# Optimization experiments

Measured on AMD Instinct MI355X. Metric: run time of the kernel, lower is better.

## Reference

```python
import jax, jax.numpy as jnp
import numpy as np

M0 = 0.3  # DTM mass parameter (layer init m0)
LIMS = [[-1.0, 1.0], [-1.0, 1.0]]
BY = 0.025


def _make_grid(lims, by):
    # Exact replica of tf_gridBy (including row ordering via full transpose)
    axes = [np.arange(lo, hi + by, by, dtype=np.float32) for lo, hi in lims]
    mesh = np.stack(np.meshgrid(*axes, indexing='ij'), 0)   # [d, n1, n2]
    grid = np.transpose(mesh).reshape(-1, len(lims))        # [N, d]
    return jnp.asarray(grid)


def setup_inputs() -> dict:
    key = jax.random.key(0)
    k1, k2 = jax.random.split(key)
    B, M = 2, 2048
    inputs = jax.random.normal(k1, (B, M, 2), dtype=jnp.float32)
    weight = jax.random.uniform(k2, (B, M), dtype=jnp.float32)  # positive weights
    grid = _make_grid(LIMS, BY)  # [6561, 2]
    return {"inputs": inputs, "weight": weight, "grid": grid}


def reference(inputs, weight, grid):
    # inputs: [B, M, d], weight: [B, M], grid: [N, d] -> dtm: [B, N]
    # Uses k = M (full sorted neighbor list); identical math to the original
    # data-dependent k = max(searchsorted)+1 truncation, since searchsorted
    # selects the same prefix index either way.
    wB = M0 * jnp.sum(weight, -1, keepdims=True)            # [B, 1] weightBound

    # Brute-force euclidean cdist grid -> points (tf_knn, r=2)
    X2 = jnp.sum(inputs * inputs, -1)                        # [B, M]
    G2 = jnp.sum(grid * grid, -1)                            # [N]
    XG = jnp.einsum('bmd,nd->bnm', inputs, grid)             # [B, N, M]
    dist = jnp.sqrt(jnp.maximum(G2[None, :, None] + X2[:, None, :] - 2.0 * XG, 0.0))

    # Full ascending sort = top_k with k=M (knnDistance, knnIndex)
    idx = jnp.argsort(dist, axis=-1)                         # [B, N, M]
    dsort = jnp.take_along_axis(dist, idx, axis=-1)

    # gather weights by neighbor index, cumulative mass
    wTemp = jnp.take_along_axis(jnp.broadcast_to(weight[:, None, :], idx.shape), idx, axis=-1)
    wcum = jnp.cumsum(wTemp, -1)                             # [B, N, M]

    bound = wB[..., None]                                    # [B, 1, 1]
    # searchsorted(side='left') == count of entries strictly below bound
    kidx = jnp.sum(wcum < bound, -1)                         # [B, N]

    d2 = dsort * dsort
    cumD = jnp.cumsum(d2 * wTemp, -1)
    val = cumD + d2 * (bound - wcum)                         # [B, N, M]
    sel = jnp.take_along_axis(val, kidx[..., None], axis=-1)[..., 0]  # [B, N]
    return jnp.sqrt(sel / wB)
```

## Files before the change

kernel.cpp:

```cpp
#include <hip/hip_runtime.h>
#include <math.h>


#define M_POINTS 2048
#define PER_LANE 32
#define M0 0.3f

template<int CTRL>
__device__ __forceinline__ float dpp_add_step(float x) {
    union { int i; float f; } u, r;
    u.f = x;
    r.i = __builtin_amdgcn_update_dpp(0, u.i, CTRL, 0xf, 0xf, true);
    return x + r.f;
}
template<int CTRL>
__device__ __forceinline__ float dpp_max_step(float x) {
    union { int i; float f; } u, r;
    u.f = x;
    r.i = __builtin_amdgcn_update_dpp(0, u.i, CTRL, 0xf, 0xf, true);
    return fmaxf(x, r.f);
}
template<int CTRL>
__device__ __forceinline__ float dpp_min_step(float x) {
    union { int i; float f; } u, r;
    u.f = x;
    r.i = __builtin_amdgcn_update_dpp(0x7F800000, u.i, CTRL, 0xf, 0xf, false);
    return fminf(x, r.f);
}
__device__ __forceinline__ float lane63(float x) {
    union { int i; float f; } u;
    u.f = x;
    u.i = __builtin_amdgcn_readlane(u.i, 63);
    return u.f;
}
__device__ __forceinline__ float wave_reduce_sum(float x) {
    x = dpp_add_step<0x111>(x); x = dpp_add_step<0x112>(x);
    x = dpp_add_step<0x114>(x); x = dpp_add_step<0x118>(x);
    x = dpp_add_step<0x142>(x); x = dpp_add_step<0x143>(x);
    return lane63(x);
}
__device__ __forceinline__ float wave_reduce_max(float x) {
    x = dpp_max_step<0x111>(x); x = dpp_max_step<0x112>(x);
    x = dpp_max_step<0x114>(x); x = dpp_max_step<0x118>(x);
    x = dpp_max_step<0x142>(x); x = dpp_max_step<0x143>(x);
    return lane63(x);
}
__device__ __forceinline__ float wave_reduce_min(float x) {
    x = dpp_min_step<0x111>(x); x = dpp_min_step<0x112>(x);
    x = dpp_min_step<0x114>(x); x = dpp_min_step<0x118>(x);
    x = dpp_min_step<0x142>(x); x = dpp_min_step<0x143>(x);
    return lane63(x);
}
__device__ __forceinline__ void wave_reduce_sum3(float& a, float& b, float& c) {
    a = dpp_add_step<0x111>(a); b = dpp_add_step<0x111>(b); c = dpp_add_step<0x111>(c);
    a = dpp_add_step<0x112>(a); b = dpp_add_step<0x112>(b); c = dpp_add_step<0x112>(c);
    a = dpp_add_step<0x114>(a); b = dpp_add_step<0x114>(b); c = dpp_add_step<0x114>(c);
    a = dpp_add_step<0x118>(a); b = dpp_add_step<0x118>(b); c = dpp_add_step<0x118>(c);
    a = dpp_add_step<0x142>(a); b = dpp_add_step<0x142>(b); c = dpp_add_step<0x142>(c);
    a = dpp_add_step<0x143>(a); b = dpp_add_step<0x143>(b); c = dpp_add_step<0x143>(c);
    a = lane63(a); b = lane63(b); c = lane63(c);
}

__global__ __launch_bounds__(256) void dtm_kernel(
    const float* __restrict__ inputs,
    const float* __restrict__ weight,
    const float* __restrict__ grid,
    float* __restrict__ out,
    int B, int N)
{
    const int lane = threadIdx.x & 63;
    const int gwave = blockIdx.x * (blockDim.x >> 6) + (threadIdx.x >> 6);
    if (gwave >= B * N) return;
    const int b = gwave / N;
    const int n = gwave - b * N;

    const float gx = grid[2 * n];
    const float gy = grid[2 * n + 1];

    const float* __restrict__ inb = inputs + (size_t)b * M_POINTS * 2;
    const float* __restrict__ wb  = weight + (size_t)b * M_POINTS;

    const int base = lane * PER_LANE;
    const float4* __restrict__ xyv = reinterpret_cast<const float4*>(inb + 2 * base);
    const float4* __restrict__ wv  = reinterpret_cast<const float4*>(wb + base);

    float d2[PER_LANE], w[PER_LANE];
    float wsum_local = 0.0f, vmax_local = 0.0f;
    #pragma unroll
    for (int q = 0; q < PER_LANE / 4; ++q) {
        const float4 wq = wv[q];
        const float4 a  = xyv[2 * q];
        const float4 c4 = xyv[2 * q + 1];
        float dx, dy;
        dx = a.x  - gx; dy = a.y  - gy; d2[4*q+0] = fmaf(dx, dx, dy * dy);
        dx = a.z  - gx; dy = a.w  - gy; d2[4*q+1] = fmaf(dx, dx, dy * dy);
        dx = c4.x - gx; dy = c4.y - gy; d2[4*q+2] = fmaf(dx, dx, dy * dy);
        dx = c4.z - gx; dy = c4.w - gy; d2[4*q+3] = fmaf(dx, dx, dy * dy);
        w[4*q+0] = wq.x; w[4*q+1] = wq.y; w[4*q+2] = wq.z; w[4*q+3] = wq.w;
        wsum_local += wq.x + wq.y + wq.z + wq.w;
        vmax_local = fmaxf(vmax_local, fmaxf(fmaxf(d2[4*q+0], d2[4*q+1]),
                                             fmaxf(d2[4*q+2], d2[4*q+3])));
    }
    const float total = wave_reduce_sum(wsum_local);
    const float vmax  = wave_reduce_max(vmax_local);
    const float bound = M0 * total;

    float vlo = 0.0f, wlo = 0.0f;
    float vhi = vmax, whi = total;
    #pragma unroll 1
    for (int pass = 0; pass < 24; ++pass) {
        if (whi - wlo <= 0.75f) break;
        const float qt = 0.25f * (vhi - vlo);
        const float t1 = vlo + qt, t2 = vlo + 2.0f * qt, t3 = vlo + 3.0f * qt;
        if (!(t1 > vlo && t1 < t2 && t2 < t3 && t3 < vhi)) break;
        float c1 = 0.0f, c2 = 0.0f, c3 = 0.0f;
        #pragma unroll
        for (int j = 0; j < PER_LANE; ++j) {
            c1 += (d2[j] <= t1) ? w[j] : 0.0f;
            c2 += (d2[j] <= t2) ? w[j] : 0.0f;
            c3 += (d2[j] <= t3) ? w[j] : 0.0f;
        }
        wave_reduce_sum3(c1, c2, c3);
        if (c1 >= bound)      { vhi = t1; whi = c1; }
        else if (c2 >= bound) { vlo = t1; wlo = c1; vhi = t2; whi = c2; }
        else if (c3 >= bound) { vlo = t2; wlo = c2; vhi = t3; whi = c3; }
        else                  { vlo = t3; wlo = c3; }
    }

    float r2 = vhi, W = wlo;
    #pragma unroll 1
    for (int step = 0; step < 64; ++step) {
        float m = __builtin_inff();
        #pragma unroll
        for (int j = 0; j < PER_LANE; ++j)
            m = fminf(m, (d2[j] > vlo) ? d2[j] : __builtin_inff());
        m = wave_reduce_min(m);
        float c = 0.0f;
        #pragma unroll
        for (int j = 0; j < PER_LANE; ++j)
            c += (d2[j] <= m) ? w[j] : 0.0f;
        c = wave_reduce_sum(c);
        if (c >= bound) { r2 = m; W = wlo; break; }
        vlo = m; wlo = c;
    }

    float S = 0.0f;
    #pragma unroll
    for (int j = 0; j < PER_LANE; ++j)
        if (d2[j] < r2) S = fmaf(w[j], d2[j], S);
    S = wave_reduce_sum(S);

    const float margin = fmaxf(bound - W, 0.0f);
    const float val = fmaxf(fmaf(r2, margin, S), 0.0f);
    if (lane == 0) out[gwave] = sqrtf(val / bound);
}

extern "C" void kernel_launch(void* const* d_in, const int* in_sizes, int n_in,
                              void* d_out, int out_size, void* d_ws, size_t ws_size,
                              hipStream_t stream) {
    const float* inputs = (const float*)d_in[0];
    const float* weight = (const float*)d_in[1];
    const float* grid   = (const float*)d_in[2];
    float* out = (float*)d_out;

    const int N = in_sizes[2] / 2;
    const int B = out_size / N;

    const int total_waves = B * N;
    const int waves_per_block = 256 / 64;
    const int blocks = (total_waves + waves_per_block - 1) / waves_per_block;

    dtm_kernel<<<blocks, 256, 0, stream>>>(inputs, weight, grid, out, B, N);
}
```

Measured before the change: 140.2 us.

## Replace quaternary threshold search with two-level LDS histogram selection

```diff
diff --git a/kernel.cpp b/kernel.cpp
--- a/kernel.cpp
+++ b/kernel.cpp
@@ -6,18 +6,18 @@
 #define PER_LANE 32
 #define M0 0.3f
 
-template<int CTRL>
+template<int CTRL, int RMASK = 0xf>
 __device__ __forceinline__ float dpp_add_step(float x) {
     union { int i; float f; } u, r;
     u.f = x;
-    r.i = __builtin_amdgcn_update_dpp(0, u.i, CTRL, 0xf, 0xf, true);
+    r.i = __builtin_amdgcn_update_dpp(0, u.i, CTRL, RMASK, 0xf, true);
     return x + r.f;
 }
 template<int CTRL>
 __device__ __forceinline__ float dpp_max_step(float x) {
     union { int i; float f; } u, r;
     u.f = x;
-    r.i = __builtin_amdgcn_update_dpp(0, u.i, CTRL, 0xf, 0xf, true);
+    r.i = __builtin_amdgcn_update_dpp(0xFF800000, u.i, CTRL, 0xf, 0xf, false);
     return fmaxf(x, r.f);
 }
 template<int CTRL>
@@ -32,6 +32,21 @@
     u.f = x;
     u.i = __builtin_amdgcn_readlane(u.i, 63);
     return u.f;
+}
+__device__ __forceinline__ float readlane_f(float x, int l) {
+    union { int i; float f; } u;
+    u.f = x;
+    u.i = __builtin_amdgcn_readlane(u.i, l);
+    return u.f;
+}
+__device__ __forceinline__ float wave_scan_sum(float x) {
+    x = dpp_add_step<0x111>(x);
+    x = dpp_add_step<0x112>(x);
+    x = dpp_add_step<0x114>(x);
+    x = dpp_add_step<0x118>(x);
+    x = dpp_add_step<0x142, 0xa>(x);
+    x = dpp_add_step<0x143, 0xc>(x);
+    return x;
 }
 __device__ __forceinline__ float wave_reduce_sum(float x) {
     x = dpp_add_step<0x111>(x); x = dpp_add_step<0x112>(x);
@@ -50,15 +65,6 @@
     x = dpp_min_step<0x114>(x); x = dpp_min_step<0x118>(x);
     x = dpp_min_step<0x142>(x); x = dpp_min_step<0x143>(x);
     return lane63(x);
-}
-__device__ __forceinline__ void wave_reduce_sum3(float& a, float& b, float& c) {
-    a = dpp_add_step<0x111>(a); b = dpp_add_step<0x111>(b); c = dpp_add_step<0x111>(c);
-    a = dpp_add_step<0x112>(a); b = dpp_add_step<0x112>(b); c = dpp_add_step<0x112>(c);
-    a = dpp_add_step<0x114>(a); b = dpp_add_step<0x114>(b); c = dpp_add_step<0x114>(c);
-    a = dpp_add_step<0x118>(a); b = dpp_add_step<0x118>(b); c = dpp_add_step<0x118>(c);
-    a = dpp_add_step<0x142>(a); b = dpp_add_step<0x142>(b); c = dpp_add_step<0x142>(c);
-    a = dpp_add_step<0x143>(a); b = dpp_add_step<0x143>(b); c = dpp_add_step<0x143>(c);
-    a = lane63(a); b = lane63(b); c = lane63(c);
 }
 
 __global__ __launch_bounds__(256) void dtm_kernel(
@@ -68,7 +74,10 @@
     float* __restrict__ out,
     int B, int N)
 {
+    __shared__ float hist[4 * 64];
     const int lane = threadIdx.x & 63;
+    float* __restrict__ hb = &hist[(threadIdx.x >> 6) * 64];
+
     const int gwave = blockIdx.x * (blockDim.x >> 6) + (threadIdx.x >> 6);
     if (gwave >= B * N) return;
     const int b = gwave / N;
@@ -105,29 +114,51 @@
     const float vmax  = wave_reduce_max(vmax_local);
     const float bound = M0 * total;
 
-    float vlo = 0.0f, wlo = 0.0f;
-    float vhi = vmax, whi = total;
-    #pragma unroll 1
-    for (int pass = 0; pass < 24; ++pass) {
-        if (whi - wlo <= 0.75f) break;
-        const float qt = 0.25f * (vhi - vlo);
-        const float t1 = vlo + qt, t2 = vlo + 2.0f * qt, t3 = vlo + 3.0f * qt;
-        if (!(t1 > vlo && t1 < t2 && t2 < t3 && t3 < vhi)) break;
-        float c1 = 0.0f, c2 = 0.0f, c3 = 0.0f;
-        #pragma unroll
-        for (int j = 0; j < PER_LANE; ++j) {
-            c1 += (d2[j] <= t1) ? w[j] : 0.0f;
-            c2 += (d2[j] <= t2) ? w[j] : 0.0f;
-            c3 += (d2[j] <= t3) ? w[j] : 0.0f;
+    const float vspan  = fmaxf(vmax, 1e-30f) * 1.0000002f;
+    const float scale1 = 64.0f / vspan;
+
+    hb[lane] = 0.0f;
+    __threadfence_block();
+    #pragma unroll
+    for (int j = 0; j < PER_LANE; ++j) {
+        const int bi = min(63, (int)(d2[j] * scale1));
+        atomicAdd(&hb[bi], w[j]);
+    }
+    __threadfence_block();
+    const float pref1 = wave_scan_sum(hb[lane]);
+    const unsigned long long m1 = __ballot(pref1 >= bound);
+    const int k = m1 ? (__ffsll((long long)m1) - 1) : 63;
+    const float wlo1 = (k == 0) ? 0.0f : readlane_f(pref1, k - 1);
+
+    hb[lane] = 0.0f;
+    __threadfence_block();
+    #pragma unroll
+    for (int j = 0; j < PER_LANE; ++j) {
+        const float x = d2[j] * scale1;
+        const int bi = min(63, (int)x);
+        if (bi == k) {
+            const int b2 = min(63, (int)((x - (float)k) * 64.0f));
+            atomicAdd(&hb[b2], w[j]);
         }
-        wave_reduce_sum3(c1, c2, c3);
-        if (c1 >= bound)      { vhi = t1; whi = c1; }
-        else if (c2 >= bound) { vlo = t1; wlo = c1; vhi = t2; whi = c2; }
-        else if (c3 >= bound) { vlo = t2; wlo = c2; vhi = t3; whi = c3; }
-        else                  { vlo = t3; wlo = c3; }
-    }
-
-    float r2 = vhi, W = wlo;
+    }
+    __threadfence_block();
+    const float pref2 = wave_scan_sum(hb[lane]);
+    const unsigned long long m2 = __ballot(wlo1 + pref2 >= bound);
+    const int k2 = m2 ? (__ffsll((long long)m2) - 1) : 63;
+    float wlo = wlo1 + ((k2 == 0) ? 0.0f : readlane_f(pref2, k2 - 1));
+
+    float cand = -1.0f;
+    #pragma unroll
+    for (int j = 0; j < PER_LANE; ++j) {
+        const float x = d2[j] * scale1;
+        const int bi = min(63, (int)x);
+        const int b2 = min(63, (int)((x - (float)k) * 64.0f));
+        const bool prior = (bi < k) || (bi == k && b2 < k2);
+        cand = prior ? fmaxf(cand, d2[j]) : cand;
+    }
+    float vlo = wave_reduce_max(cand);
+
+    float r2 = vmax, W = wlo;
     #pragma unroll 1
     for (int step = 0; step < 64; ++step) {
         float m = __builtin_inff();
```

Result: slower. 218.6 us (+55.9%).
